# Kernel tuning notes

Measured on AMD Instinct MI355X. Metric: run time of the kernel, lower is better.

## Reference

```python
import jax, jax.numpy as jnp
import numpy as np

N = 8192
IN_F = 128
OUT_F = 128
ALPHA = 0.2  # LeakyReLU negative slope
NEG_INF = -9e15


def setup_inputs() -> dict:
    key = jax.random.key(0)
    k1, k2, k3, k4 = jax.random.split(key, 4)
    h = jax.random.normal(k1, (N, IN_F), dtype=jnp.float32)
    adj = jax.random.randint(k2, (N, N), 0, 2, dtype=jnp.int32)
    # nn.Linear(in, out, bias=False).weight is (out, in); store as (in, out) for h @ W
    W = jax.random.normal(k3, (IN_F, OUT_F), dtype=jnp.float32) * (1.0 / np.sqrt(IN_F))
    # a: (2*out_features, 1), xavier_uniform with gain=1.414
    limit = 1.414 * np.sqrt(6.0 / (2 * OUT_F + 1))
    a = jax.random.uniform(k4, (2 * OUT_F, 1), dtype=jnp.float32, minval=-limit, maxval=limit)
    return {"h": h, "adj": adj, "W": W, "a": a}


def reference(h, adj, W, a):
    Wh = h @ W  # (N, OUT_F)
    a1 = a[:OUT_F, 0]   # score contribution from source node i
    a2 = a[OUT_F:, 0]   # score contribution from target node j
    # e_ij = leakyrelu(Wh_i . a1 + Wh_j . a2) -- avoids the O(N^2 * 2F) concat
    s1 = Wh @ a1  # (N,)
    s2 = Wh @ a2  # (N,)
    e = jax.nn.leaky_relu(s1[:, None] + s2[None, :], negative_slope=ALPHA)  # (N, N)
    masked = jnp.where(adj > 0, e, NEG_INF)
    attention = jax.nn.softmax(masked, axis=1)  # (N, N)
    # dropout is a no-op in eval mode
    h_prime = attention @ Wh  # (N, OUT_F)
    return jax.nn.elu(h_prime)  # concat=True -> ELU
```

## Files before the change

### kernel.cpp

```cpp
#include <hip/hip_runtime.h>
#include <cstdint>
#include <cstddef>


#define NROW 8192
#define FDIM 128

typedef _Float16 f16;
typedef f16 f16x8 __attribute__((ext_vector_type(8)));
typedef float f32x4 __attribute__((ext_vector_type(4)));

#define WS_WHT 0u
#define WS_BP  (2u*1024u*1024u)
#define WS_S12 (4u*1024u*1024u)
#define WS_K12 (WS_S12 + 64u*1024u)
#define WS_EF  (WS_K12 + 64u*1024u)
#define WS_M2  (WS_EF + 64u*1024u)
#define WS_PWS (WS_M2 + 4u*1024u)

__global__ __launch_bounds__(256) void k1_wh(const float* __restrict__ h,
                                             const float* __restrict__ W,
                                             f16* __restrict__ WhT,
                                             f16* __restrict__ Bp,
                                             unsigned* __restrict__ M2key) {
  __shared__ float hT[128 * 36];
  const int t = (int)threadIdx.x;
  const int rb = (int)blockIdx.x * 32;
  if (blockIdx.x == 0 && t == 0) *M2key = 0u;
  const f32x4* hv = (const f32x4*)(h + (size_t)rb * FDIM);
#pragma unroll
  for (int i = 0; i < 4; ++i) {
    int fidx = t + i * 256;
    f32x4 v = hv[fidx];
    int e0 = fidx * 4;
    int r = e0 >> 7, k = e0 & 127;
    hT[(k + 0) * 36 + r] = v[0];
    hT[(k + 1) * 36 + r] = v[1];
    hT[(k + 2) * 36 + r] = v[2];
    hT[(k + 3) * 36 + r] = v[3];
  }
  __syncthreads();
  const int f = t & 127, rh = t >> 7;
  f32x4 z = {0.f, 0.f, 0.f, 0.f};
  f32x4 acc0 = z, acc1 = z, acc2 = z, acc3 = z;
  for (int k = 0; k < 128; ++k) {
    float w = W[k * FDIM + f];
    const f32x4* hp = (const f32x4*)(hT + k * 36 + rh * 16);
    acc0 += hp[0] * w;
    acc1 += hp[1] * w;
    acc2 += hp[2] * w;
    acc3 += hp[3] * w;
  }
  union { f16 hx[16]; uint4 u[2]; } pk;
#pragma unroll
  for (int q = 0; q < 4; ++q) {
    pk.hx[0 + q]  = (f16)acc0[q];
    pk.hx[4 + q]  = (f16)acc1[q];
    pk.hx[8 + q]  = (f16)acc2[q];
    pk.hx[12 + q] = (f16)acc3[q];
  }
  uint4* dst = (uint4*)(WhT + (size_t)f * NROW + rb + rh * 16);
  dst[0] = pk.u[0];
  dst[1] = pk.u[1];
  f16* bdst = Bp + (size_t)blockIdx.x * 4096 + (size_t)(f >> 4) * 512
                 + (size_t)(2 * rh) * 128 + (size_t)(f & 15) * 8;
  *(uint4*)bdst = pk.u[0];
  *(uint4*)(bdst + 128) = pk.u[1];
}

__global__ __launch_bounds__(256) void k1b_s(const f16* __restrict__ WhT,
                                             const float* __restrict__ a,
                                             float2* __restrict__ s12,
                                             unsigned* __restrict__ M2key) {
  __shared__ float part[2][4][64];
  const int l = (int)threadIdx.x & 63;
  const int fc = (int)threadIdx.x >> 6;
  const int r = (int)blockIdx.x * 64 + l;
  float s1 = 0.f, s2 = 0.f;
  for (int f = fc * 32; f < fc * 32 + 32; ++f) {
    float w = (float)WhT[(size_t)f * NROW + r];
    s1 = fmaf(w, a[f], s1);
    s2 = fmaf(w, a[128 + f], s2);
  }
  part[0][fc][l] = s1;
  part[1][fc][l] = s2;
  __syncthreads();
  if (fc == 0) {
    s1 = part[0][0][l] + part[0][1][l] + part[0][2][l] + part[0][3][l];
    s2 = part[1][0][l] + part[1][1][l] + part[1][2][l] + part[1][3][l];
    s12[r] = make_float2(s1, s2);
    float mx = s2;
#pragma unroll
    for (int off = 32; off; off >>= 1) mx = fmaxf(mx, __shfl_xor(mx, off, 64));
    if (l == 0) {
      unsigned key = __float_as_uint(mx);
      key = (key & 0x80000000u) ? ~key : (key | 0x80000000u);
      atomicMax(M2key, key);
    }
  }
}

__global__ __launch_bounds__(256) void k1c_prep(const float2* __restrict__ s12,
                                                const unsigned* __restrict__ M2key,
                                                float2* __restrict__ K12,
                                                float2* __restrict__ EF) {
  int j = (int)blockIdx.x * 256 + (int)threadIdx.x;
  unsigned key = *M2key;
  float M2 = (key & 0x80000000u) ? __uint_as_float(key ^ 0x80000000u)
                                 : __uint_as_float(~key);
  float2 s = s12[j];
  float c = s.x + M2;
  c = fmaxf(c, 0.2f * c);
  K12[j] = make_float2(__expf(s.x - c), __expf(0.2f * s.x - c));
  EF[j] = make_float2(__expf(s.y), __expf(0.2f * s.y));
}

__global__ __launch_bounds__(256) void k2_main(const int* __restrict__ adj,
                                               const f16* __restrict__ Bp,
                                               const float2* __restrict__ K12,
                                               const float* __restrict__ EF,
                                               float* __restrict__ Pws,
                                               float* __restrict__ Dws,
                                               int jspan) {
  const int tid = (int)threadIdx.x;
  const int L = tid & 63, w = tid >> 6;
  const int wid = (int)blockIdx.x * 4 + w;
  const int rg = wid & 511;
  const int c = wid >> 9;
  const int rb = rg * 16;
  const int m = L & 15, kq = L >> 4;
  const int row = rb + m;
  const int j0 = c * jspan;
  const int niter = jspan >> 5;

  const float2 kk = K12[row];
  const float kap1 = kk.x, kap2 = kk.y;

  const int* ap = adj + (size_t)row * NROW + j0 + kq * 8;
  const float* ep = EF ? (EF + 2 * (size_t)(j0 + kq * 8)) : EF;
  const f16* bp = Bp + (size_t)(j0 >> 5) * 4096 + (size_t)L * 8;

  int4 A[4][2];
#pragma unroll
  for (int s = 0; s < 4; ++s) {
    A[s][0] = *(const int4*)(ap + s * 32);
    A[s][1] = *(const int4*)(ap + s * 32 + 4);
  }
  f32x4 E[4];
#pragma unroll
  for (int q = 0; q < 4; ++q) E[q] = *(const f32x4*)(ep + q * 4);

  f32x4 z = {0.f, 0.f, 0.f, 0.f};
  f32x4 acc[8] = {z, z, z, z, z, z, z, z};
  float dloc = 0.f;

  for (int ii = 0; ii < niter; ii += 4) {
#pragma unroll
    for (int s = 0; s < 4; ++s) {
      const int it = ii + s;
      const f16* bt = bp + (size_t)it * 4096;
      f16x8 B0 = *(const f16x8*)(bt);
      f16x8 B1 = *(const f16x8*)(bt + 512);
      f16x8 B2 = *(const f16x8*)(bt + 1024);
      f16x8 B3 = *(const f16x8*)(bt + 1536);
      f16x8 B4 = *(const f16x8*)(bt + 2048);
      f16x8 B5 = *(const f16x8*)(bt + 2560);
      f16x8 B6 = *(const f16x8*)(bt + 3072);
      f16x8 B7 = *(const f16x8*)(bt + 3584);

      f16x8 af;
      {
        const int4 a0 = A[s][0], a1 = A[s][1];
        float p;
        p = fmaxf(E[0][0] * kap1, E[0][1] * kap2); p = (a0.x > 0) ? p : 0.f; dloc += p; af[0] = (f16)p;
        p = fmaxf(E[0][2] * kap1, E[0][3] * kap2); p = (a0.y > 0) ? p : 0.f; dloc += p; af[1] = (f16)p;
        p = fmaxf(E[1][0] * kap1, E[1][1] * kap2); p = (a0.z > 0) ? p : 0.f; dloc += p; af[2] = (f16)p;
        p = fmaxf(E[1][2] * kap1, E[1][3] * kap2); p = (a0.w > 0) ? p : 0.f; dloc += p; af[3] = (f16)p;
        p = fmaxf(E[2][0] * kap1, E[2][1] * kap2); p = (a1.x > 0) ? p : 0.f; dloc += p; af[4] = (f16)p;
        p = fmaxf(E[2][2] * kap1, E[2][3] * kap2); p = (a1.y > 0) ? p : 0.f; dloc += p; af[5] = (f16)p;
        p = fmaxf(E[3][0] * kap1, E[3][1] * kap2); p = (a1.z > 0) ? p : 0.f; dloc += p; af[6] = (f16)p;
        p = fmaxf(E[3][2] * kap1, E[3][3] * kap2); p = (a1.w > 0) ? p : 0.f; dloc += p; af[7] = (f16)p;
      }

      {
        const int itn = (it + 4 < niter) ? it + 4 : it;
        A[s][0] = *(const int4*)(ap + itn * 32);
        A[s][1] = *(const int4*)(ap + itn * 32 + 4);
      }
      {
        const int itn = (it + 1 < niter) ? it + 1 : it;
#pragma unroll
        for (int q = 0; q < 4; ++q) E[q] = *(const f32x4*)(ep + itn * 64 + q * 4);
      }

      acc[0] = __builtin_amdgcn_mfma_f32_16x16x32_f16(af, B0, acc[0], 0, 0, 0);
      acc[1] = __builtin_amdgcn_mfma_f32_16x16x32_f16(af, B1, acc[1], 0, 0, 0);
      acc[2] = __builtin_amdgcn_mfma_f32_16x16x32_f16(af, B2, acc[2], 0, 0, 0);
      acc[3] = __builtin_amdgcn_mfma_f32_16x16x32_f16(af, B3, acc[3], 0, 0, 0);
      acc[4] = __builtin_amdgcn_mfma_f32_16x16x32_f16(af, B4, acc[4], 0, 0, 0);
      acc[5] = __builtin_amdgcn_mfma_f32_16x16x32_f16(af, B5, acc[5], 0, 0, 0);
      acc[6] = __builtin_amdgcn_mfma_f32_16x16x32_f16(af, B6, acc[6], 0, 0, 0);
      acc[7] = __builtin_amdgcn_mfma_f32_16x16x32_f16(af, B7, acc[7], 0, 0, 0);
    }
  }

  dloc += __shfl_xor(dloc, 16, 64);
  dloc += __shfl_xor(dloc, 32, 64);
  if (L < 16) Dws[(size_t)c * NROW + rb + L] = dloc;

  float* P = Pws + ((size_t)c * NROW + rb) * FDIM + (L & 15);
#pragma unroll
  for (int nt = 0; nt < 8; ++nt) {
#pragma unroll
    for (int reg = 0; reg < 4; ++reg) {
      int rr = kq * 4 + reg;
      P[(size_t)rr * FDIM + nt * 16] = acc[nt][reg];
    }
  }
}

__global__ __launch_bounds__(256) void k3_comb(const float* __restrict__ Pws,
                                               const float* __restrict__ Dws,
                                               float* __restrict__ out, int S) {
  int g = (int)blockIdx.x * 256 + (int)threadIdx.x;
  int r = g >> 5, f4 = g & 31;
  f32x4 s = {0.f, 0.f, 0.f, 0.f};
  float den = 0.f;
  for (int c2 = 0; c2 < S; ++c2) {
    s += *(const f32x4*)(Pws + ((size_t)c2 * NROW + r) * FDIM + f4 * 4);
    den += Dws[(size_t)c2 * NROW + r];
  }
  float inv = 1.0f / den;
  f32x4 o;
#pragma unroll
  for (int e = 0; e < 4; ++e) {
    float x = s[e] * inv;
    o[e] = x > 0.f ? x : expm1f(x);
  }
  *(f32x4*)(out + (size_t)r * FDIM + f4 * 4) = o;
}

extern "C" void kernel_launch(void* const* d_in, const int* in_sizes, int n_in,
                              void* d_out, int out_size, void* d_ws, size_t ws_size,
                              hipStream_t stream) {
  const float* h = (const float*)d_in[0];
  const int* adj = (const int*)d_in[1];
  const float* W = (const float*)d_in[2];
  const float* a = (const float*)d_in[3];
  float* out = (float*)d_out;
  char* ws = (char*)d_ws;
  f16* WhT = (f16*)(ws + WS_WHT);
  f16* Bp = (f16*)(ws + WS_BP);
  float2* s12 = (float2*)(ws + WS_S12);
  float2* K12 = (float2*)(ws + WS_K12);
  float2* EF = (float2*)(ws + WS_EF);
  unsigned* M2 = (unsigned*)(ws + WS_M2);

  const size_t partial_bytes = (size_t)NROW * FDIM * 4;
  int S = (ws_size >= WS_PWS + 8 * partial_bytes + 8 * NROW * 4) ? 8 : 2;
  float* Pws = (float*)(ws + WS_PWS);
  float* Dws = (float*)(ws + WS_PWS + (size_t)S * partial_bytes);
  int jspan = NROW / S;

  k1_wh<<<dim3(256), dim3(256), 0, stream>>>(h, W, WhT, Bp, M2);
  k1b_s<<<dim3(128), dim3(256), 0, stream>>>(WhT, a, s12, M2);
  k1c_prep<<<dim3(32), dim3(256), 0, stream>>>(s12, M2, K12, EF);
  k2_main<<<dim3(128 * S), dim3(256), 0, stream>>>(adj, Bp, K12, (const float*)EF, Pws, Dws, jspan);
  k3_comb<<<dim3(1024), dim3(256), 0, stream>>>(Pws, Dws, out, S);
}
```

Measured before the change: 477.2 us.

## Compute attention weights in packed fp16 and get row sums from an extra MFMA

```diff
diff --git a/kernel.cpp b/kernel.cpp
--- a/kernel.cpp
+++ b/kernel.cpp
@@ -103,22 +103,24 @@
 __global__ __launch_bounds__(256) void k1c_prep(const float2* __restrict__ s12,
                                                 const unsigned* __restrict__ M2key,
                                                 float2* __restrict__ K12,
-                                                float2* __restrict__ EF) {
+                                                f16* __restrict__ Eh,
+                                                f16* __restrict__ Fh) {
   int j = (int)blockIdx.x * 256 + (int)threadIdx.x;
   unsigned key = *M2key;
   float M2 = (key & 0x80000000u) ? __uint_as_float(key ^ 0x80000000u)
                                  : __uint_as_float(~key);
   float2 s = s12[j];
-  float c = s.x + M2;
-  c = fmaxf(c, 0.2f * c);
-  K12[j] = make_float2(__expf(s.x - c), __expf(0.2f * s.x - c));
-  EF[j] = make_float2(__expf(s.y), __expf(0.2f * s.y));
+  float u = s.x + M2;
+  K12[j] = make_float2(__expf(fminf(0.f, 0.8f * u)), __expf(-0.8f * fmaxf(u, 0.f)));
+  Eh[j] = (f16)__expf(s.y - M2);
+  Fh[j] = (f16)__expf(0.2f * (s.y - M2));
 }
 
 __global__ __launch_bounds__(256) void k2_main(const int* __restrict__ adj,
                                                const f16* __restrict__ Bp,
                                                const float2* __restrict__ K12,
-                                               const float* __restrict__ EF,
+                                               const f16* __restrict__ Eh,
+                                               const f16* __restrict__ Fh,
                                                float* __restrict__ Pws,
                                                float* __restrict__ Dws,
                                                int jspan) {
@@ -134,29 +136,36 @@
   const int niter = jspan >> 5;
 
   const float2 kk = K12[row];
-  const float kap1 = kk.x, kap2 = kk.y;
+  f16x8 kap1v, kap2v, bones;
+#pragma unroll
+  for (int i = 0; i < 8; ++i) {
+    kap1v[i] = (f16)kk.x;
+    kap2v[i] = (f16)kk.y;
+    bones[i] = (f16)1.0f;
+  }
 
   const int* ap = adj + (size_t)row * NROW + j0 + kq * 8;
-  const float* ep = EF ? (EF + 2 * (size_t)(j0 + kq * 8)) : EF;
+  const f16* ehp = Eh + j0 + kq * 8;
+  const f16* fhp = Fh + j0 + kq * 8;
   const f16* bp = Bp + (size_t)(j0 >> 5) * 4096 + (size_t)L * 8;
 
-  int4 A[4][2];
-#pragma unroll
-  for (int s = 0; s < 4; ++s) {
-    A[s][0] = *(const int4*)(ap + s * 32);
-    A[s][1] = *(const int4*)(ap + s * 32 + 4);
-  }
-  f32x4 E[4];
-#pragma unroll
-  for (int q = 0; q < 4; ++q) E[q] = *(const f32x4*)(ep + q * 4);
+  int4 A0s[2], A1s[2];
+  f16x8 Er[2], Fr[2];
+#pragma unroll
+  for (int s = 0; s < 2; ++s) {
+    A0s[s] = *(const int4*)(ap + s * 32);
+    A1s[s] = *(const int4*)(ap + s * 32 + 4);
+    Er[s] = *(const f16x8*)(ehp + s * 32);
+    Fr[s] = *(const f16x8*)(fhp + s * 32);
+  }
 
   f32x4 z = {0.f, 0.f, 0.f, 0.f};
   f32x4 acc[8] = {z, z, z, z, z, z, z, z};
-  float dloc = 0.f;
-
-  for (int ii = 0; ii < niter; ii += 4) {
-#pragma unroll
-    for (int s = 0; s < 4; ++s) {
+  f32x4 accd = z;
+
+  for (int ii = 0; ii < niter; ii += 2) {
+#pragma unroll
+    for (int s = 0; s < 2; ++s) {
       const int it = ii + s;
       const f16* bt = bp + (size_t)it * 4096;
       f16x8 B0 = *(const f16x8*)(bt);
@@ -168,30 +177,25 @@
       f16x8 B6 = *(const f16x8*)(bt + 3072);
       f16x8 B7 = *(const f16x8*)(bt + 3584);
 
+      f16x8 t = __builtin_elementwise_max(Er[s] * kap1v, Fr[s] * kap2v);
       f16x8 af;
       {
-        const int4 a0 = A[s][0], a1 = A[s][1];
-        float p;
-        p = fmaxf(E[0][0] * kap1, E[0][1] * kap2); p = (a0.x > 0) ? p : 0.f; dloc += p; af[0] = (f16)p;
-        p = fmaxf(E[0][2] * kap1, E[0][3] * kap2); p = (a0.y > 0) ? p : 0.f; dloc += p; af[1] = (f16)p;
-        p = fmaxf(E[1][0] * kap1, E[1][1] * kap2); p = (a0.z > 0) ? p : 0.f; dloc += p; af[2] = (f16)p;
-        p = fmaxf(E[1][2] * kap1, E[1][3] * kap2); p = (a0.w > 0) ? p : 0.f; dloc += p; af[3] = (f16)p;
-        p = fmaxf(E[2][0] * kap1, E[2][1] * kap2); p = (a1.x > 0) ? p : 0.f; dloc += p; af[4] = (f16)p;
-        p = fmaxf(E[2][2] * kap1, E[2][3] * kap2); p = (a1.y > 0) ? p : 0.f; dloc += p; af[5] = (f16)p;
-        p = fmaxf(E[3][0] * kap1, E[3][1] * kap2); p = (a1.z > 0) ? p : 0.f; dloc += p; af[6] = (f16)p;
-        p = fmaxf(E[3][2] * kap1, E[3][3] * kap2); p = (a1.w > 0) ? p : 0.f; dloc += p; af[7] = (f16)p;
+        const int4 a0 = A0s[s], a1 = A1s[s];
+        af[0] = (a0.x > 0) ? t[0] : (f16)0.f;
+        af[1] = (a0.y > 0) ? t[1] : (f16)0.f;
+        af[2] = (a0.z > 0) ? t[2] : (f16)0.f;
+        af[3] = (a0.w > 0) ? t[3] : (f16)0.f;
+        af[4] = (a1.x > 0) ? t[4] : (f16)0.f;
+        af[5] = (a1.y > 0) ? t[5] : (f16)0.f;
+        af[6] = (a1.z > 0) ? t[6] : (f16)0.f;
+        af[7] = (a1.w > 0) ? t[7] : (f16)0.f;
       }
 
-      {
-        const int itn = (it + 4 < niter) ? it + 4 : it;
-        A[s][0] = *(const int4*)(ap + itn * 32);
-        A[s][1] = *(const int4*)(ap + itn * 32 + 4);
-      }
-      {
-        const int itn = (it + 1 < niter) ? it + 1 : it;
-#pragma unroll
-        for (int q = 0; q < 4; ++q) E[q] = *(const f32x4*)(ep + itn * 64 + q * 4);
-      }
+      const int itn = (it + 2 < niter) ? it + 2 : it;
+      Er[s] = *(const f16x8*)(ehp + itn * 32);
+      Fr[s] = *(const f16x8*)(fhp + itn * 32);
+      A0s[s] = *(const int4*)(ap + itn * 32);
+      A1s[s] = *(const int4*)(ap + itn * 32 + 4);
 
       acc[0] = __builtin_amdgcn_mfma_f32_16x16x32_f16(af, B0, acc[0], 0, 0, 0);
       acc[1] = __builtin_amdgcn_mfma_f32_16x16x32_f16(af, B1, acc[1], 0, 0, 0);
@@ -201,14 +205,17 @@
       acc[5] = __builtin_amdgcn_mfma_f32_16x16x32_f16(af, B5, acc[5], 0, 0, 0);
       acc[6] = __builtin_amdgcn_mfma_f32_16x16x32_f16(af, B6, acc[6], 0, 0, 0);
       acc[7] = __builtin_amdgcn_mfma_f32_16x16x32_f16(af, B7, acc[7], 0, 0, 0);
+      accd = __builtin_amdgcn_mfma_f32_16x16x32_f16(af, bones, accd, 0, 0, 0);
     }
   }
 
-  dloc += __shfl_xor(dloc, 16, 64);
-  dloc += __shfl_xor(dloc, 32, 64);
-  if (L < 16) Dws[(size_t)c * NROW + rb + L] = dloc;
-
-  float* P = Pws + ((size_t)c * NROW + rb) * FDIM + (L & 15);
+  if (m == 0) {
+#pragma unroll
+    for (int reg = 0; reg < 4; ++reg)
+      Dws[(size_t)c * NROW + rb + kq * 4 + reg] = accd[reg];
+  }
+
+  float* P = Pws + ((size_t)c * NROW + rb) * FDIM + m;
 #pragma unroll
   for (int nt = 0; nt < 8; ++nt) {
 #pragma unroll
@@ -253,7 +260,8 @@
   f16* Bp = (f16*)(ws + WS_BP);
   float2* s12 = (float2*)(ws + WS_S12);
   float2* K12 = (float2*)(ws + WS_K12);
-  float2* EF = (float2*)(ws + WS_EF);
+  f16* Eh = (f16*)(ws + WS_EF);
+  f16* Fh = (f16*)(ws + WS_EF + 16u * 1024u);
   unsigned* M2 = (unsigned*)(ws + WS_M2);
 
   const size_t partial_bytes = (size_t)NROW * FDIM * 4;
@@ -264,7 +272,7 @@
 
   k1_wh<<<dim3(256), dim3(256), 0, stream>>>(h, W, WhT, Bp, M2);
   k1b_s<<<dim3(128), dim3(256), 0, stream>>>(WhT, a, s12, M2);
-  k1c_prep<<<dim3(32), dim3(256), 0, stream>>>(s12, M2, K12, EF);
-  k2_main<<<dim3(128 * S), dim3(256), 0, stream>>>(adj, Bp, K12, (const float*)EF, Pws, Dws, jspan);
+  k1c_prep<<<dim3(32), dim3(256), 0, stream>>>(s12, M2, K12, Eh, Fh);
+  k2_main<<<dim3(128 * S), dim3(256), 0, stream>>>(adj, Bp, K12, Eh, Fh, Pws, Dws, jspan);
   k3_comb<<<dim3(1024), dim3(256), 0, stream>>>(Pws, Dws, out, S);
 }
```

New measurement: 470.3 us. Within noise of the previous version (-1.4%).
